# Kernel optimization log

Hardware: AMD Instinct MI355X
Metric: run time of the kernel (lower is better)

Reference implementation:

```python
import jax, jax.numpy as jnp
import numpy as np

EPS = 1e-5

def _ln(x, g, b):
    m = jnp.mean(x, -1, keepdims=True)
    v = jnp.mean((x - m) ** 2, -1, keepdims=True)
    return (x - m) * jax.lax.rsqrt(v + EPS) * g + b

def _lstm(x, Wih, Whh, bih, bhh):
    # x: [B, T, D]; torch gate order i, f, g, o; h0 = c0 = 0
    B = x.shape[0]
    H = Whh.shape[1]
    h0 = jnp.zeros((B, H), x.dtype)
    c0 = jnp.zeros((B, H), x.dtype)
    bias = bih + bhh
    def step(carry, xt):
        h, c = carry
        gates = xt @ Wih.T + h @ Whh.T + bias  # [B, 4H]
        i, f, g, o = jnp.split(gates, 4, axis=-1)
        c = jax.nn.sigmoid(f) * c + jax.nn.sigmoid(i) * jnp.tanh(g)
        h = jax.nn.sigmoid(o) * jnp.tanh(c)
        return (h, c), h
    _, hs = jax.lax.scan(step, (h0, c0), jnp.swapaxes(x, 0, 1))
    return jnp.swapaxes(hs, 0, 1)  # [B, T, H]

def setup_inputs() -> dict:
    key = jax.random.key(0)
    ks = jax.random.split(key, 20)
    N, C, F, T = 4, 64, 256, 256
    D, H = 128, 32  # LSTM in/out
    s = 0.05
    inp = {
        "inputs": jax.random.normal(ks[0], (N, C, F, T, 2), jnp.float32),
        "ln1_g": jnp.ones((D,), jnp.float32), "ln1_b": jnp.zeros((D,), jnp.float32),
        "Wih_q": s * jax.random.normal(ks[1], (4 * H, D), jnp.float32),
        "Whh_q": s * jax.random.normal(ks[2], (4 * H, H), jnp.float32),
        "bih_q": s * jax.random.normal(ks[3], (4 * H,), jnp.float32),
        "bhh_q": s * jax.random.normal(ks[4], (4 * H,), jnp.float32),
        "Wih_k": s * jax.random.normal(ks[5], (4 * H, D), jnp.float32),
        "Whh_k": s * jax.random.normal(ks[6], (4 * H, H), jnp.float32),
        "bih_k": s * jax.random.normal(ks[7], (4 * H,), jnp.float32),
        "bhh_k": s * jax.random.normal(ks[8], (4 * H,), jnp.float32),
        "Wih_v": s * jax.random.normal(ks[9], (4 * H, D), jnp.float32),
        "Whh_v": s * jax.random.normal(ks[10], (4 * H, H), jnp.float32),
        "bih_v": s * jax.random.normal(ks[11], (4 * H,), jnp.float32),
        "bhh_v": s * jax.random.normal(ks[12], (4 * H,), jnp.float32),
        "ln2_g": jnp.ones((H,), jnp.float32), "ln2_b": jnp.zeros((H,), jnp.float32),
        "Wr": s * jax.random.normal(ks[13], (C, H // 2), jnp.float32),
        "br": s * jax.random.normal(ks[14], (C,), jnp.float32),
        "Wi": s * jax.random.normal(ks[15], (C, H // 2), jnp.float32),
        "bi": s * jax.random.normal(ks[16], (C,), jnp.float32),
        "ln3_g": jnp.ones((C,), jnp.float32), "ln3_b": jnp.zeros((C,), jnp.float32),
        "prelu_a": jnp.full((1,), 0.25, jnp.float32),
    }
    return inp

def reference(inputs, ln1_g, ln1_b,
              Wih_q, Whh_q, bih_q, bhh_q,
              Wih_k, Whh_k, bih_k, bhh_k,
              Wih_v, Whh_v, bih_v, bhh_v,
              ln2_g, ln2_b, Wr, br, Wi, bi,
              ln3_g, ln3_b, prelu_a):
    N, C, F, T, ri = inputs.shape
    # [N,C,F,T,2] -> [N*F, T, C, 2] -> concat real/imag -> [N*F, T, 2C]
    x4 = jnp.transpose(inputs, (0, 2, 3, 1, 4)).reshape(N * F, T, C, ri)
    x = jnp.concatenate([x4[..., 0], x4[..., 1]], axis=-1)  # [B, T, 128]
    # Self_Attention_T_RICAT (single head)
    xn = _ln(x, ln1_g, ln1_b)
    q = _lstm(xn, Wih_q, Whh_q, bih_q, bhh_q)  # [B, T, 32]
    k = _lstm(xn, Wih_k, Whh_k, bih_k, bhh_k)
    v = _lstm(xn, Wih_v, Whh_v, bih_v, bhh_v)
    energy = jnp.einsum('btf,bsf->bts', q, k) / 4.0  # / 16**0.5
    mask = jnp.tril(jnp.ones((T, T), x.dtype))
    attn = jax.nn.softmax(energy * mask, axis=-1)  # multiplicative mask, as in source
    wv = jnp.einsum('bts,bsf->btf', attn, v)  # [B, T, 32]
    out = _ln(wv, ln2_g, ln2_b)
    # complex-valued linear fusion
    xr, xi = jnp.split(out, 2, axis=-1)  # [B, T, 16] each
    lr_r = xr @ Wr.T + br
    li_i = xi @ Wi.T + bi
    lr_i = xi @ Wr.T + br
    li_r = xr @ Wi.T + bi
    out_real = (lr_r - li_i).reshape(N, F, T, C).transpose(0, 3, 1, 2)  # [N,C,F,T]
    out_imag = (lr_i + li_r).reshape(N, F, T, C).transpose(0, 3, 1, 2)
    outs = jnp.stack([out_real, out_imag], axis=-1)  # [N,C,F,T,2]
    outs_t = jnp.swapaxes(outs, 1, 4)  # [N,2,F,T,C]
    outs = jnp.swapaxes(_ln(outs_t, ln3_g, ln3_b), 1, 4)
    outs = jnp.where(outs >= 0, outs, prelu_a[0] * outs)  # PReLU (eval mode, dropout=identity)
    return outs + inputs
```

## Files before the change

### kernel.cpp

```cpp
#include <hip/hip_runtime.h>
#include <hip/hip_bf16.h>
#include <stddef.h>


typedef __bf16 bf16x8 __attribute__((ext_vector_type(8)));
typedef float f32x4 __attribute__((ext_vector_type(4)));
typedef _Float16 f16x2 __attribute__((ext_vector_type(2)));
typedef _Float16 f16x8 __attribute__((ext_vector_type(8)));

__device__ __forceinline__ ushort f2bf(float x) {
    uint u = __builtin_bit_cast(uint, x);
    uint r = (u + 0x7fffu + ((u >> 16) & 1u)) >> 16;
    return (ushort)r;
}
__device__ __forceinline__ float bflo2f(uint v) {
    return __builtin_bit_cast(float, v << 16);
}
__device__ __forceinline__ float bfhi2f(uint v) {
    return __builtin_bit_cast(float, v & 0xffff0000u);
}

__device__ __forceinline__ float fsig(float x) {
    return __builtin_amdgcn_rcpf(1.f + __expf(-x));
}
__device__ __forceinline__ float ftanh(float x) {
    return 1.f - 2.f * __builtin_amdgcn_rcpf(__expf(2.f * x) + 1.f);
}
__device__ __forceinline__ float fdot2(f16x2 a, f16x2 b, float c) {
#if __has_builtin(__builtin_amdgcn_fdot2)
    return __builtin_amdgcn_fdot2(a, b, c, false);
#else
    return c + (float)a.x * (float)b.x + (float)a.y * (float)b.y;
#endif
}
__device__ __forceinline__ float wredsum(float v) {
#pragma unroll
    for (int off = 32; off; off >>= 1) v += __shfl_xor(v, off);
    return v;
}
__device__ __forceinline__ float hredsum(float v) {
#pragma unroll
    for (int off = 16; off; off >>= 1) v += __shfl_xor(v, off);
    return v;
}

__global__ __launch_bounds__(256) void k_prep(const float* __restrict__ in,
                                              const float* __restrict__ g1,
                                              const float* __restrict__ b1,
                                              ushort* __restrict__ xn) {
    __shared__ float xl[32][129];
    const int n = blockIdx.z, f = blockIdx.y, t0 = blockIdx.x * 32;
    const int tid = threadIdx.x;
    const int c = tid >> 2, q = tid & 3;
    const float* src = in + ((size_t)(n * 64 + c) * 256 + f) * 512 + t0 * 2 + q * 16;
#pragma unroll
    for (int e = 0; e < 4; ++e) {
        float4 v4 = *(const float4*)(src + e * 4);
        int dt = q * 8 + e * 2;
        xl[dt][c]          = v4.x;
        xl[dt][c + 64]     = v4.y;
        xl[dt + 1][c]      = v4.z;
        xl[dt + 1][c + 64] = v4.w;
    }
    __syncthreads();
    const int lane = tid & 63, w = tid >> 6;
    const int b = n * 256 + f;
#pragma unroll 1
    for (int r = 0; r < 8; ++r) {
        int dt = w * 8 + r;
        float a = xl[dt][lane], bb = xl[dt][lane + 64];
        float s = wredsum(a + bb);
        float mean = s * 0.0078125f;
        float da = a - mean, db = bb - mean;
        float var = wredsum(da * da + db * db) * 0.0078125f;
        float inv = __builtin_amdgcn_rsqf(var + 1e-5f);
        size_t base = ((size_t)b * 256 + (t0 + dt)) * 128;
        xn[base + lane]      = f2bf(da * inv * g1[lane] + b1[lane]);
        xn[base + lane + 64] = f2bf(db * inv * g1[lane + 64] + b1[lane + 64]);
    }
}

__global__ __launch_bounds__(256) void k_gemm(const ushort* __restrict__ xn,
                                              const float* __restrict__ Wq,
                                              const float* __restrict__ Wk,
                                              const float* __restrict__ Wv,
                                              const float* __restrict__ bihq, const float* __restrict__ bhhq,
                                              const float* __restrict__ bihk, const float* __restrict__ bhhk,
                                              const float* __restrict__ bihv, const float* __restrict__ bhhv,
                                              ushort* __restrict__ gx) {
    __shared__ ushort a_lds[128 * 136];
    __shared__ ushort w_lds[64 * 136];
    const int tid = threadIdx.x;
    const int m0 = blockIdx.x * 128;
    const int yb = blockIdx.y;
    const int l = yb >> 1, n0 = (yb & 1) * 64;
    const float* W   = (l == 0) ? Wq   : (l == 1) ? Wk   : Wv;
    const float* bih = (l == 0) ? bihq : (l == 1) ? bihk : bihv;
    const float* bhh = (l == 0) ? bhhq : (l == 1) ? bhhk : bhhv;

#pragma unroll
    for (int p = 0; p < 8; ++p) {
        int idx = p * 256 + tid;
        int r = idx >> 4, c = idx & 15;
        uint4 v = *(const uint4*)(xn + (size_t)(m0 + r) * 128 + c * 8);
        *(uint4*)&a_lds[r * 136 + c * 8] = v;
    }
#pragma unroll
    for (int p = 0; p < 4; ++p) {
        int idx = p * 256 + tid;
        int r = idx >> 4, c = idx & 15;
        const float* wp = W + (size_t)(n0 + r) * 128 + c * 8;
        float4 wa = *(const float4*)wp;
        float4 wb = *(const float4*)(wp + 4);
        union { ushort u[8]; uint4 v; } pk;
        pk.u[0] = f2bf(wa.x); pk.u[1] = f2bf(wa.y); pk.u[2] = f2bf(wa.z); pk.u[3] = f2bf(wa.w);
        pk.u[4] = f2bf(wb.x); pk.u[5] = f2bf(wb.y); pk.u[6] = f2bf(wb.z); pk.u[7] = f2bf(wb.w);
        *(uint4*)&w_lds[r * 136 + c * 8] = pk.v;
    }
    __syncthreads();

    const int w = tid >> 6, lane = tid & 63;
    const int wr = w >> 1, wc = w & 1;
    const int row16 = lane & 15, koct = lane >> 4;

    f32x4 acc[4][2];
#pragma unroll
    for (int mi = 0; mi < 4; ++mi)
#pragma unroll
        for (int ni = 0; ni < 2; ++ni) acc[mi][ni] = (f32x4){0.f, 0.f, 0.f, 0.f};

#pragma unroll
    for (int ki = 0; ki < 4; ++ki) {
        bf16x8 af[4], bfr[2];
#pragma unroll
        for (int mi = 0; mi < 4; ++mi)
            af[mi] = *(const bf16x8*)&a_lds[(wr * 64 + mi * 16 + row16) * 136 + ki * 32 + koct * 8];
#pragma unroll
        for (int ni = 0; ni < 2; ++ni)
            bfr[ni] = *(const bf16x8*)&w_lds[(wc * 32 + ni * 16 + row16) * 136 + ki * 32 + koct * 8];
#pragma unroll
        for (int mi = 0; mi < 4; ++mi)
#pragma unroll
            for (int ni = 0; ni < 2; ++ni)
                acc[mi][ni] = __builtin_amdgcn_mfma_f32_16x16x32_bf16(af[mi], bfr[ni], acc[mi][ni], 0, 0, 0);
    }

    float bs[2];
#pragma unroll
    for (int ni = 0; ni < 2; ++ni) {
        int ncol = n0 + wc * 32 + ni * 16 + row16;
        bs[ni] = bih[ncol] + bhh[ncol];
    }
#pragma unroll
    for (int mi = 0; mi < 4; ++mi)
#pragma unroll
        for (int ni = 0; ni < 2; ++ni) {
            int ncol = n0 + wc * 32 + ni * 16 + row16;
            int pos = (ncol & 64) | ((ncol >> 5) & 1) | (2 * (ncol & 31));
#pragma unroll
            for (int q = 0; q < 4; ++q) {
                size_t m = (size_t)m0 + wr * 64 + mi * 16 + koct * 4 + q;
                gx[m * 384 + l * 128 + pos] = f2bf(acc[mi][ni][q] + bs[ni]);
            }
        }
}

__global__ __launch_bounds__(256) void k_lstm(const ushort* __restrict__ gx,
                                              const float* __restrict__ Whq,
                                              const float* __restrict__ Whk,
                                              const float* __restrict__ Whv,
                                              ushort* __restrict__ qkv) {
    __shared__ _Float16 hbuf[4][64];
    const int tid = threadIdx.x, w = tid >> 6, lane = tid & 63;
    const int j = lane & 31, hl = lane >> 5;
    const int sid = blockIdx.x * 4 + w;
    const int l = sid >> 10, b = sid & 1023;
    const float* Wh = (l == 0) ? Whq : (l == 1) ? Whk : Whv;
    const int rowA = hl * 64 + j;
    const int rowB = rowA + 32;
    f16x2 wA[16], wB[16];
    {
        const float* pA = Wh + (size_t)rowA * 32;
        const float* pB = Wh + (size_t)rowB * 32;
#pragma unroll
        for (int e = 0; e < 16; ++e) {
            wA[e] = f16x2{(_Float16)pA[2 * e], (_Float16)pA[2 * e + 1]};
            wB[e] = f16x2{(_Float16)pB[2 * e], (_Float16)pB[2 * e + 1]};
        }
    }
    hbuf[w][lane] = (_Float16)0.f;
    float c = 0.f;
    const ushort* gp = gx + (size_t)b * 98304 + l * 128 + hl * 64 + 2 * j;
    ushort* outp = qkv + (size_t)sid * 8192;
    uint gc = *(const uint*)gp;
    uint gn = *(const uint*)(gp + 384);
    for (int t = 0; t < 256; ++t) {
        uint g2v = 0;
        if (t + 2 < 256) g2v = *(const uint*)(gp + (size_t)(t + 2) * 384);
        union { f16x8 v[4]; f16x2 d[16]; } hh;
        const f16x8* hp = (const f16x8*)&hbuf[w][hl * 32];
#pragma unroll
        for (int e = 0; e < 4; ++e) hh.v[e] = hp[e];
        float a0 = 0.f, a1 = 0.f;
#pragma unroll
        for (int e = 0; e < 16; ++e) {
            a0 = fdot2(hh.d[e], wA[e], a0);
            a1 = fdot2(hh.d[e], wB[e], a1);
        }
        float g0 = bflo2f(gc) + a0;
        float g1 = bfhi2f(gc) + a1;
        float xg0 = __shfl_xor(g0, 32);
        float xg1 = __shfl_xor(g1, 32);
        float gi = hl ? xg0 : g0;
        float gf = hl ? xg1 : g1;
        float gg = hl ? g0 : xg0;
        float go = hl ? g1 : xg1;
        c = fsig(gf) * c + fsig(gi) * ftanh(gg);
        float hN = fsig(go) * ftanh(c);
        hbuf[w][hl * 32 + j] = (_Float16)hN;
        if (hl == 0) outp[(size_t)t * 32 + j] = f2bf(hN);
        gc = gn; gn = g2v;
    }
}

__global__ __launch_bounds__(256) void k_attn(const ushort* __restrict__ qkvb,
                                              float* __restrict__ wvout) {
    __shared__ ushort k_sw[256 * 32];
    __shared__ ushort vt_sw[32 * 256];
    __shared__ ushort p_sw[4][16 * 256];
    const int tid = threadIdx.x, w = tid >> 6, lane = tid & 63;
    const int b = blockIdx.x;
    const ushort* qb = qkvb + (size_t)b * 8192;
    const ushort* kb = qkvb + 8388608 + (size_t)b * 8192;
    const ushort* vb = qkvb + 16777216 + (size_t)b * 8192;
#pragma unroll
    for (int p = 0; p < 4; ++p) {
        int idx = p * 256 + tid;
        int s = idx >> 2, cc = idx & 3;
        uint4 kv = *(const uint4*)(kb + s * 32 + cc * 8);
        int cK = cc ^ ((s >> 1) & 3);
        *(uint4*)&k_sw[s * 32 + cK * 8] = kv;
        uint4 vv = *(const uint4*)(vb + s * 32 + cc * 8);
        union { uint4 v; ushort u[8]; } un; un.v = vv;
#pragma unroll
        for (int e = 0; e < 8; ++e) {
            int row = cc * 8 + e;
            vt_sw[row * 256 + (((s >> 3) ^ (row & 7)) << 3) + (s & 7)] = un.u[e];
        }
    }
    __syncthreads();
    const int r16 = lane & 15, koct = lane >> 4;
    ushort* pw = p_sw[w];
    bf16x8 qf[4];
#pragma unroll
    for (int i = 0; i < 4; ++i) {
        int t = (w * 4 + i) * 16 + r16;
        qf[i] = *(const bf16x8*)(qb + t * 32 + koct * 8);
    }
#pragma unroll 1
    for (int i = 0; i < 4; ++i) {
        const int tb = (w * 4 + i) * 16;
        f32x4 acc[16];
#pragma unroll
        for (int st = 0; st < 16; ++st) acc[st] = (f32x4){0.f, 0.f, 0.f, 0.f};
#pragma unroll
        for (int st = 0; st < 16; ++st) {
            int s = st * 16 + r16;
            int cK = koct ^ ((s >> 1) & 3);
            bf16x8 kf = *(const bf16x8*)&k_sw[s * 32 + cK * 8];
            acc[st] = __builtin_amdgcn_mfma_f32_16x16x32_bf16(qf[i], kf, acc[st], 0, 0, 0);
        }
        float mx[4] = {-1e30f, -1e30f, -1e30f, -1e30f};
#pragma unroll
        for (int st = 0; st < 16; ++st) {
            int s = st * 16 + r16;
#pragma unroll
            for (int q = 0; q < 4; ++q) {
                int t = tb + koct * 4 + q;
                float v = (s <= t) ? acc[st][q] * 0.25f : 0.f;
                acc[st][q] = v;
                mx[q] = fmaxf(mx[q], v);
            }
        }
#pragma unroll
        for (int off = 1; off < 16; off <<= 1)
#pragma unroll
            for (int q = 0; q < 4; ++q) mx[q] = fmaxf(mx[q], __shfl_xor(mx[q], off));
        float sm[4] = {0.f, 0.f, 0.f, 0.f};
#pragma unroll
        for (int st = 0; st < 16; ++st)
#pragma unroll
            for (int q = 0; q < 4; ++q) {
                float p = __expf(acc[st][q] - mx[q]);
                acc[st][q] = p; sm[q] += p;
            }
#pragma unroll
        for (int off = 1; off < 16; off <<= 1)
#pragma unroll
            for (int q = 0; q < 4; ++q) sm[q] += __shfl_xor(sm[q], off);
        float rs[4];
#pragma unroll
        for (int q = 0; q < 4; ++q) rs[q] = __builtin_amdgcn_rcpf(sm[q]);
#pragma unroll
        for (int st = 0; st < 16; ++st) {
            int schunk = st * 2 + (r16 >> 3), sl = r16 & 7;
#pragma unroll
            for (int q = 0; q < 4; ++q) {
                int tl = koct * 4 + q;
                pw[tl * 256 + ((schunk ^ (tl & 7)) << 3) + sl] = f2bf(acc[st][q] * rs[q]);
            }
        }
        __asm__ volatile("s_waitcnt lgkmcnt(0)" ::: "memory");
        f32x4 oa[2];
        oa[0] = (f32x4){0.f, 0.f, 0.f, 0.f};
        oa[1] = (f32x4){0.f, 0.f, 0.f, 0.f};
#pragma unroll
        for (int ks = 0; ks < 8; ++ks) {
            int kc = ks * 4 + koct;
            bf16x8 pa = *(const bf16x8*)&pw[r16 * 256 + ((kc ^ (r16 & 7)) << 3)];
#pragma unroll
            for (int n = 0; n < 2; ++n) {
                int row = n * 16 + r16;
                bf16x8 vf = *(const bf16x8*)&vt_sw[row * 256 + ((kc ^ (row & 7)) << 3)];
                oa[n] = __builtin_amdgcn_mfma_f32_16x16x32_bf16(pa, vf, oa[n], 0, 0, 0);
            }
        }
#pragma unroll
        for (int n = 0; n < 2; ++n)
#pragma unroll
            for (int q = 0; q < 4; ++q)
                wvout[((size_t)b * 256 + tb + koct * 4 + q) * 32 + n * 16 + r16] = oa[n][q];
    }
}

__global__ __launch_bounds__(256) void k_post(const float* __restrict__ wv,
                                              const float* __restrict__ in,
                                              const float* __restrict__ g2,
                                              const float* __restrict__ b2,
                                              const float* __restrict__ Wr,
                                              const float* __restrict__ br,
                                              const float* __restrict__ Wi,
                                              const float* __restrict__ bi,
                                              const float* __restrict__ g3,
                                              const float* __restrict__ b3,
                                              const float* __restrict__ pa,
                                              float* __restrict__ outp) {
    __shared__ float xv[32][33];
    __shared__ float wr_l[64][17], wi_l[64][17];
    __shared__ float out_s[64][65];
    const int tid = threadIdx.x;
    const int n = blockIdx.z, f = blockIdx.y, t0 = blockIdx.x * 32;
    const int b = n * 256 + f;
    for (int idx = tid; idx < 1024; idx += 256) {
        int dt = idx >> 5, j = idx & 31;
        xv[dt][j] = wv[((size_t)b * 256 + t0 + dt) * 32 + j];
        int cc = idx >> 4, jjj = idx & 15;
        wr_l[cc][jjj] = Wr[idx];
        wi_l[cc][jjj] = Wi[idx];
    }
    __syncthreads();
    const int lane = tid & 63, w = tid >> 6;
#pragma unroll 1
    for (int r = 0; r < 4; ++r) {
        int dt = w * 8 + r * 2 + (lane >> 5);
        int j = lane & 31;
        float v = xv[dt][j];
        float mean = hredsum(v) * 0.03125f;
        float d = v - mean;
        float var = hredsum(d * d) * 0.03125f;
        float inv = __builtin_amdgcn_rsqf(var + 1e-5f);
        xv[dt][j] = d * inv * g2[j] + b2[j];
    }
    __syncthreads();
    const int c = lane;
    const float g3c = g3[c], b3c = b3[c];
    const float bd = br[c] - bi[c], bsum = br[c] + bi[c];
    const float alpha = pa[0];
#pragma unroll 1
    for (int r = 0; r < 8; ++r) {
        int dt = w * 8 + r;
        float re = 0.f, im = 0.f;
#pragma unroll
        for (int j = 0; j < 16; ++j) {
            float xr = xv[dt][j], xi2 = xv[dt][16 + j];
            float wrv = wr_l[c][j], wiv = wi_l[c][j];
            re += xr * wrv; re -= xi2 * wiv;
            im += xi2 * wrv; im += xr * wiv;
        }
        re += bd; im += bsum;
        float mR = wredsum(re) * 0.015625f;
        float dR = re - mR;
        float vR = wredsum(dR * dR) * 0.015625f;
        float nR = dR * __builtin_amdgcn_rsqf(vR + 1e-5f) * g3c + b3c;
        nR = (nR >= 0.f) ? nR : alpha * nR;
        float mI = wredsum(im) * 0.015625f;
        float dI = im - mI;
        float vI = wredsum(dI * dI) * 0.015625f;
        float nI = dI * __builtin_amdgcn_rsqf(vI + 1e-5f) * g3c + b3c;
        nI = (nI >= 0.f) ? nI : alpha * nI;
        out_s[c][dt * 2]     = nR;
        out_s[c][dt * 2 + 1] = nI;
    }
    __syncthreads();
    const int cc = tid >> 2, q = tid & 3;
    size_t base = ((size_t)(n * 64 + cc) * 256 + f) * 512 + t0 * 2 + q * 16;
#pragma unroll
    for (int e = 0; e < 4; ++e) {
        float4 iv = *(const float4*)(in + base + e * 4);
        int k0 = q * 16 + e * 4;
        float4 ov;
        ov.x = out_s[cc][k0]     + iv.x;
        ov.y = out_s[cc][k0 + 1] + iv.y;
        ov.z = out_s[cc][k0 + 2] + iv.z;
        ov.w = out_s[cc][k0 + 3] + iv.w;
        *(float4*)(outp + base + e * 4) = ov;
    }
}

extern "C" void kernel_launch(void* const* d_in, const int* in_sizes, int n_in,
                              void* d_out, int out_size, void* d_ws, size_t ws_size,
                              hipStream_t stream) {
    const float* in   = (const float*)d_in[0];
    const float* g1   = (const float*)d_in[1];
    const float* b1   = (const float*)d_in[2];
    const float* Wq   = (const float*)d_in[3];
    const float* Whq  = (const float*)d_in[4];
    const float* bihq = (const float*)d_in[5];
    const float* bhhq = (const float*)d_in[6];
    const float* Wk   = (const float*)d_in[7];
    const float* Whk  = (const float*)d_in[8];
    const float* bihk = (const float*)d_in[9];
    const float* bhhk = (const float*)d_in[10];
    const float* Wv   = (const float*)d_in[11];
    const float* Whv  = (const float*)d_in[12];
    const float* bihv = (const float*)d_in[13];
    const float* bhhv = (const float*)d_in[14];
    const float* g2   = (const float*)d_in[15];
    const float* b2   = (const float*)d_in[16];
    const float* Wr   = (const float*)d_in[17];
    const float* br   = (const float*)d_in[18];
    const float* Wi   = (const float*)d_in[19];
    const float* bi   = (const float*)d_in[20];
    const float* g3   = (const float*)d_in[21];
    const float* b3   = (const float*)d_in[22];
    const float* pa   = (const float*)d_in[23];
    float* outp = (float*)d_out;

    ushort* gxb  = (ushort*)d_ws;
    ushort* xnb  = (ushort*)((char*)d_ws + 201326592);
    ushort* qkvb = (ushort*)((char*)d_ws + 268435456);
    float*  wvb  = (float*)((char*)d_ws + 318767104);

    k_prep<<<dim3(8, 256, 4), dim3(256), 0, stream>>>(in, g1, b1, xnb);
    k_gemm<<<dim3(2048, 6), dim3(256), 0, stream>>>(xnb, Wq, Wk, Wv,
                                                    bihq, bhhq, bihk, bhhk, bihv, bhhv, gxb);
    k_lstm<<<dim3(768), dim3(256), 0, stream>>>(gxb, Whq, Whk, Whv, qkvb);
    k_attn<<<dim3(1024), dim3(256), 0, stream>>>(qkvb, wvb);
    k_post<<<dim3(8, 256, 4), dim3(256), 0, stream>>>(wvb, in, g2, b2,
                                                      Wr, br, Wi, bi, g3, b3, pa, outp);
}
```

Measured before the change: 555.6 us.

## Batch LSTM recurrence across 16 sequences with bf16 MFMA per step

The LSTM kernel now processes 16 sequences per block. Each timestep's recurrent matmul (h @ Whh^T) runs as four 16x16x32 bf16 MFMAs with the precomputed input gates as accumulators, replacing per-lane fp16 dot2 loops over one sequence per wave. The gate layout written by the GEMM kernel is permuted to match the MFMA output fragment, and h is double-buffered in LDS with a block barrier each step. This cuts the serial instruction count per step, but recurrent weights and hidden state drop from fp16 to bf16, and the grid shrinks to 192 blocks of 128 threads, which lowers occupancy.

```diff
diff --git a/kernel.cpp b/kernel.cpp
--- a/kernel.cpp
+++ b/kernel.cpp
@@ -5,33 +5,18 @@
 
 typedef __bf16 bf16x8 __attribute__((ext_vector_type(8)));
 typedef float f32x4 __attribute__((ext_vector_type(4)));
-typedef _Float16 f16x2 __attribute__((ext_vector_type(2)));
-typedef _Float16 f16x8 __attribute__((ext_vector_type(8)));
 
 __device__ __forceinline__ ushort f2bf(float x) {
     uint u = __builtin_bit_cast(uint, x);
     uint r = (u + 0x7fffu + ((u >> 16) & 1u)) >> 16;
     return (ushort)r;
 }
-__device__ __forceinline__ float bflo2f(uint v) {
-    return __builtin_bit_cast(float, v << 16);
-}
-__device__ __forceinline__ float bfhi2f(uint v) {
-    return __builtin_bit_cast(float, v & 0xffff0000u);
-}
 
 __device__ __forceinline__ float fsig(float x) {
     return __builtin_amdgcn_rcpf(1.f + __expf(-x));
 }
 __device__ __forceinline__ float ftanh(float x) {
     return 1.f - 2.f * __builtin_amdgcn_rcpf(__expf(2.f * x) + 1.f);
-}
-__device__ __forceinline__ float fdot2(f16x2 a, f16x2 b, float c) {
-#if __has_builtin(__builtin_amdgcn_fdot2)
-    return __builtin_amdgcn_fdot2(a, b, c, false);
-#else
-    return c + (float)a.x * (float)b.x + (float)a.y * (float)b.y;
-#endif
 }
 __device__ __forceinline__ float wredsum(float v) {
 #pragma unroll
@@ -156,7 +141,7 @@
 #pragma unroll
         for (int ni = 0; ni < 2; ++ni) {
             int ncol = n0 + wc * 32 + ni * 16 + row16;
-            int pos = (ncol & 64) | ((ncol >> 5) & 1) | (2 * (ncol & 31));
+            int pos = ((ncol & 31) << 2) | (ncol >> 5);
 #pragma unroll
             for (int q = 0; q < 4; ++q) {
                 size_t m = (size_t)m0 + wr * 64 + mi * 16 + koct * 4 + q;
@@ -165,61 +150,79 @@
         }
 }
 
-__global__ __launch_bounds__(256) void k_lstm(const ushort* __restrict__ gx,
+__global__ __launch_bounds__(128) void k_lstm(const ushort* __restrict__ gx,
                                               const float* __restrict__ Whq,
                                               const float* __restrict__ Whk,
                                               const float* __restrict__ Whv,
                                               ushort* __restrict__ qkv) {
-    __shared__ _Float16 hbuf[4][64];
+    __shared__ ushort H[2][16][40];
     const int tid = threadIdx.x, w = tid >> 6, lane = tid & 63;
-    const int j = lane & 31, hl = lane >> 5;
-    const int sid = blockIdx.x * 4 + w;
-    const int l = sid >> 10, b = sid & 1023;
+    const int r16 = lane & 15, koct = lane >> 4;
+    const int l = blockIdx.x >> 6, bgrp = blockIdx.x & 63;
+    const int b = bgrp * 16 + r16;
     const float* Wh = (l == 0) ? Whq : (l == 1) ? Whk : Whv;
-    const int rowA = hl * 64 + j;
-    const int rowB = rowA + 32;
-    f16x2 wA[16], wB[16];
-    {
-        const float* pA = Wh + (size_t)rowA * 32;
-        const float* pB = Wh + (size_t)rowB * 32;
-#pragma unroll
-        for (int e = 0; e < 16; ++e) {
-            wA[e] = f16x2{(_Float16)pA[2 * e], (_Float16)pA[2 * e + 1]};
-            wB[e] = f16x2{(_Float16)pB[2 * e], (_Float16)pB[2 * e + 1]};
-        }
-    }
-    hbuf[w][lane] = (_Float16)0.f;
-    float c = 0.f;
-    const ushort* gp = gx + (size_t)b * 98304 + l * 128 + hl * 64 + 2 * j;
-    ushort* outp = qkv + (size_t)sid * 8192;
-    uint gc = *(const uint*)gp;
-    uint gn = *(const uint*)(gp + 384);
+    bf16x8 wf[4];
+#pragma unroll
+    for (int gidx = 0; gidx < 4; ++gidx) {
+        int grow = (gidx * 2 + w) * 16 + r16;
+        const float* wp = Wh + (size_t)grow * 32 + koct * 8;
+        float4 wa = *(const float4*)wp;
+        float4 wb2 = *(const float4*)(wp + 4);
+        union { ushort u[8]; bf16x8 v; } pk;
+        pk.u[0] = f2bf(wa.x);  pk.u[1] = f2bf(wa.y);  pk.u[2] = f2bf(wa.z);  pk.u[3] = f2bf(wa.w);
+        pk.u[4] = f2bf(wb2.x); pk.u[5] = f2bf(wb2.y); pk.u[6] = f2bf(wb2.z); pk.u[7] = f2bf(wb2.w);
+        wf[gidx] = pk.v;
+    }
+    for (int i = tid; i < 640; i += 128) ((ushort*)H[0])[i] = 0;
+    __syncthreads();
+    const char* gbase = (const char*)gx + (size_t)(b * 256) * 768 + l * 256 + w * 128 + koct * 32;
+    uint4 pf[2][2];
+#pragma unroll
+    for (int tt = 0; tt < 2; ++tt) {
+        pf[tt][0] = *(const uint4*)(gbase + (size_t)tt * 768);
+        pf[tt][1] = *(const uint4*)(gbase + (size_t)tt * 768 + 16);
+    }
+    float c4[4] = {0.f, 0.f, 0.f, 0.f};
+    const int j0 = w * 16 + koct * 4;
+    ushort* outp = qkv + ((size_t)(l * 1024 + b)) * 8192 + j0;
+#pragma unroll 2
     for (int t = 0; t < 256; ++t) {
-        uint g2v = 0;
-        if (t + 2 < 256) g2v = *(const uint*)(gp + (size_t)(t + 2) * 384);
-        union { f16x8 v[4]; f16x2 d[16]; } hh;
-        const f16x8* hp = (const f16x8*)&hbuf[w][hl * 32];
-#pragma unroll
-        for (int e = 0; e < 4; ++e) hh.v[e] = hp[e];
-        float a0 = 0.f, a1 = 0.f;
-#pragma unroll
-        for (int e = 0; e < 16; ++e) {
-            a0 = fdot2(hh.d[e], wA[e], a0);
-            a1 = fdot2(hh.d[e], wB[e], a1);
-        }
-        float g0 = bflo2f(gc) + a0;
-        float g1 = bfhi2f(gc) + a1;
-        float xg0 = __shfl_xor(g0, 32);
-        float xg1 = __shfl_xor(g1, 32);
-        float gi = hl ? xg0 : g0;
-        float gf = hl ? xg1 : g1;
-        float gg = hl ? g0 : xg0;
-        float go = hl ? g1 : xg1;
-        c = fsig(gf) * c + fsig(gi) * ftanh(gg);
-        float hN = fsig(go) * ftanh(c);
-        hbuf[w][hl * 32 + j] = (_Float16)hN;
-        if (hl == 0) outp[(size_t)t * 32 + j] = f2bf(hN);
-        gc = gn; gn = g2v;
+        const int rb = t & 1, wbuf = (t + 1) & 1;
+        bf16x8 hf = *(const bf16x8*)&H[rb][r16][koct * 8];
+        uint4 ca = pf[t & 1][0], cb = pf[t & 1][1];
+        {
+            int tn = (t + 2 < 256) ? t + 2 : 255;
+            pf[t & 1][0] = *(const uint4*)(gbase + (size_t)tn * 768);
+            pf[t & 1][1] = *(const uint4*)(gbase + (size_t)tn * 768 + 16);
+        }
+        uint eu[8] = {ca.x, ca.y, ca.z, ca.w, cb.x, cb.y, cb.z, cb.w};
+        f32x4 acc[4];
+#pragma unroll
+        for (int gidx = 0; gidx < 4; ++gidx) {
+#pragma unroll
+            for (int q = 0; q < 4; ++q) {
+                int e = 4 * q + gidx;
+                uint u = eu[e >> 1];
+                uint bfv = (e & 1) ? (u & 0xffff0000u) : (u << 16);
+                acc[gidx][q] = __builtin_bit_cast(float, bfv);
+            }
+        }
+#pragma unroll
+        for (int gidx = 0; gidx < 4; ++gidx)
+            acc[gidx] = __builtin_amdgcn_mfma_f32_16x16x32_bf16(wf[gidx], hf, acc[gidx], 0, 0, 0);
+        ushort hu[4];
+#pragma unroll
+        for (int q = 0; q < 4; ++q) {
+            float gi = acc[0][q], gf = acc[1][q], gg = acc[2][q], go = acc[3][q];
+            float cN = fsig(gf) * c4[q] + fsig(gi) * ftanh(gg);
+            c4[q] = cN;
+            hu[q] = f2bf(fsig(go) * ftanh(cN));
+        }
+        uint2 hp = make_uint2((uint)hu[0] | ((uint)hu[1] << 16),
+                              (uint)hu[2] | ((uint)hu[3] << 16));
+        *(uint2*)&H[wbuf][r16][j0] = hp;
+        *(uint2*)(outp + (size_t)t * 32) = hp;
+        __syncthreads();
     }
 }
 
@@ -454,7 +457,7 @@
     k_prep<<<dim3(8, 256, 4), dim3(256), 0, stream>>>(in, g1, b1, xnb);
     k_gemm<<<dim3(2048, 6), dim3(256), 0, stream>>>(xnb, Wq, Wk, Wv,
                                                     bihq, bhhq, bihk, bhhk, bihv, bhhv, gxb);
-    k_lstm<<<dim3(768), dim3(256), 0, stream>>>(gxb, Whq, Whk, Whv, qkvb);
+    k_lstm<<<dim3(192), dim3(128), 0, stream>>>(gxb, Whq, Whk, Whv, qkvb);
     k_attn<<<dim3(1024), dim3(256), 0, stream>>>(qkvb, wvb);
     k_post<<<dim3(8, 256, 4), dim3(256), 0, stream>>>(wvb, in, g2, b2,
                                                       Wr, br, Wi, bi, g3, b3, pa, outp);
```

Result: slower. 573.8 us (+3.3%).
